# Kernel tuning notes

Hardware: AMD Instinct MI355X
Metric: run time of the kernel (lower is better)

## Reference

```python
import jax, jax.numpy as jnp
import numpy as np

H = 256  # GRU hidden size
V = 56   # decoder vocab / fc1 out


def gru_cell(x, h, wih, whh, bih, bhh):
    # PyTorch GRU cell math (gate order: r, z, n)
    gi = x @ wih.T + bih
    gh = h @ whh.T + bhh
    ir, iz, inn = jnp.split(gi, 3, axis=-1)
    hr, hz, hn = jnp.split(gh, 3, axis=-1)
    r = jax.nn.sigmoid(ir + hr)
    z = jax.nn.sigmoid(iz + hz)
    n = jnp.tanh(inn + r * hn)
    return (1.0 - z) * n + z * h


def gru_scan(seq, h0, wih, whh, bih, bhh):
    def step(h, xt):
        h = gru_cell(xt, h, wih, whh, bih, bhh)
        return h, h
    hT, ys = jax.lax.scan(step, h0, seq)
    return ys, hT


def bigru(seq, pf, pb):
    # seq: (S, N, F). Returns (S, N, 2H), final fwd hidden (N,H), final bwd hidden (N,H)
    S, N, _ = seq.shape
    h0 = jnp.zeros((N, H), seq.dtype)
    yf, hf = gru_scan(seq, h0, *pf)
    yb_rev, hb = gru_scan(seq[::-1], h0, *pb)
    return jnp.concatenate([yf, yb_rev[::-1]], axis=-1), hf, hb


def setup_inputs() -> dict:
    key = jax.random.key(0)
    ks = iter(jax.random.split(key, 32))
    s = 0.05
    p = {}
    p["x"] = jax.random.normal(next(ks), (64, 48, 512, 2, 2), dtype=jnp.float32)
    # bi_gru_1: input 192
    for d in ("f", "b"):
        p[f"w_ih_1{d}"] = jax.random.normal(next(ks), (3 * H, 192), jnp.float32) * s
        p[f"w_hh_1{d}"] = jax.random.normal(next(ks), (3 * H, H), jnp.float32) * s
        p[f"b_ih_1{d}"] = jax.random.normal(next(ks), (3 * H,), jnp.float32) * s
        p[f"b_hh_1{d}"] = jax.random.normal(next(ks), (3 * H,), jnp.float32) * s
    # bi_gru_2: input 512
    for d in ("f", "b"):
        p[f"w_ih_2{d}"] = jax.random.normal(next(ks), (3 * H, 2 * H), jnp.float32) * s
        p[f"w_hh_2{d}"] = jax.random.normal(next(ks), (3 * H, H), jnp.float32) * s
        p[f"b_ih_2{d}"] = jax.random.normal(next(ks), (3 * H,), jnp.float32) * s
        p[f"b_hh_2{d}"] = jax.random.normal(next(ks), (3 * H,), jnp.float32) * s
    # decoder GRU: input 56
    p["w_ih_d"] = jax.random.normal(next(ks), (3 * H, V), jnp.float32) * s
    p["w_hh_d"] = jax.random.normal(next(ks), (3 * H, H), jnp.float32) * s
    p["b_ih_d"] = jax.random.normal(next(ks), (3 * H,), jnp.float32) * s
    p["b_hh_d"] = jax.random.normal(next(ks), (3 * H,), jnp.float32) * s
    p["w_fc1"] = jax.random.normal(next(ks), (V, H), jnp.float32) * s
    p["b_fc1"] = jax.random.normal(next(ks), (V,), jnp.float32) * s
    p["w_adj"] = jax.random.normal(next(ks), (H, 2 * H), jnp.float32) * s
    p["b_adj"] = jax.random.normal(next(ks), (H,), jnp.float32) * s
    p["target_length"] = 6
    return p


def reference(x,
              w_ih_1f, w_hh_1f, b_ih_1f, b_hh_1f,
              w_ih_1b, w_hh_1b, b_ih_1b, b_hh_1b,
              w_ih_2f, w_hh_2f, b_ih_2f, b_hh_2f,
              w_ih_2b, w_hh_2b, b_ih_2b, b_hh_2b,
              w_ih_d, w_hh_d, b_ih_d, b_hh_d,
              w_fc1, b_fc1, w_adj, b_adj,
              target_length):
    B, C, T, Hh, Ww = x.shape
    # permute(2,0,1,3,4).contiguous().view(B, T, -1): flat buffer in (T,B,..) order reshaped to (B,T,feat)
    seq = jnp.transpose(x, (2, 0, 1, 3, 4)).reshape(B, T, C * Hh * Ww)
    # GRUs run seq-first: seq dim = B, batch dim = T (faithful to the torch code)
    y1, _, _ = bigru(seq, (w_ih_1f, w_hh_1f, b_ih_1f, b_hh_1f),
                     (w_ih_1b, w_hh_1b, b_ih_1b, b_hh_1b))
    # dropout is identity at inference
    y2, hf, hb = bigru(y1, (w_ih_2f, w_hh_2f, b_ih_2f, b_hh_2f),
                       (w_ih_2b, w_hh_2b, b_ih_2b, b_hh_2b))
    combined = jnp.concatenate([hf, hb], axis=-1)       # (T, 2H)
    dec_h_all = combined @ w_adj.T + b_adj              # (T, H)
    dec_h = dec_h_all[:B]                               # loop over b in range(B) selects first B rows
    inp0 = jnp.zeros((B, V), x.dtype)

    def step(carry, _):
        inp, h = carry
        h = gru_cell(inp, h, w_ih_d, w_hh_d, b_ih_d, b_hh_d)
        out = h @ w_fc1.T + b_fc1
        return (out, h), out

    _, outs = jax.lax.scan(step, (inp0, dec_h), None, length=target_length)
    return jnp.transpose(outs, (1, 0, 2))  # (B, target_length, V)
```

## Files before the change

### kernel.cpp

```cpp
#include <hip/hip_runtime.h>
#include <hip/hip_fp16.h>
#include <stdint.h>


#define HD 256
#define G3 768
#define NSEQ 64
#define NSTEP 64

typedef _Float16 hvec2 __attribute__((ext_vector_type(2)));
typedef _Float16 f16x8 __attribute__((ext_vector_type(8)));
typedef float f32x4 __attribute__((ext_vector_type(4)));

__device__ __forceinline__ float sigmf(float x) {
    return 1.0f / (1.0f + __expf(-x));
}

#if __has_builtin(__builtin_amdgcn_fdot2)
__device__ __forceinline__ float fdot2u(uint32_t w, uint32_t h, float acc) {
    return __builtin_amdgcn_fdot2(__builtin_bit_cast(hvec2, w),
                                  __builtin_bit_cast(hvec2, h), acc, false);
}
#else
__device__ __forceinline__ float fdot2u(uint32_t w, uint32_t h, float acc) {
    const __half2 wv = __builtin_bit_cast(__half2, w);
    const __half2 hv = __builtin_bit_cast(__half2, h);
    acc += __half2float(wv.x) * __half2float(hv.x);
    acc += __half2float(wv.y) * __half2float(hv.y);
    return acc;
}
#endif

__device__ __forceinline__ uint32_t pkh(float a, float b) {
    uint32_t lo = __half_as_ushort(__float2half_rn(a));
    uint32_t hi = __half_as_ushort(__float2half_rn(b));
    return lo | (hi << 16);
}

#define L8(X) X(0) X(1) X(2) X(3) X(4) X(5) X(6) X(7)

#define LRES(i) \
    const uint4 wr##i = wbase[(i) * G3]; \
    const uint4 wz##i = wbase[(i) * G3 + 256]; \
    const uint4 wn##i = wbase[(i) * G3 + 512];

#define DRES(i) { \
    const uint4 hp = *(const uint4*)&hb[hoff + 4 * (i)]; \
    ar0 = fdot2u(wr##i.x, hp.x, ar0); ar1 = fdot2u(wr##i.y, hp.y, ar1); \
    ar0 = fdot2u(wr##i.z, hp.z, ar0); ar1 = fdot2u(wr##i.w, hp.w, ar1); \
    az0 = fdot2u(wz##i.x, hp.x, az0); az1 = fdot2u(wz##i.y, hp.y, az1); \
    az0 = fdot2u(wz##i.z, hp.z, az0); az1 = fdot2u(wz##i.w, hp.w, az1); \
    an0 = fdot2u(wn##i.x, hp.x, an0); an1 = fdot2u(wn##i.y, hp.y, an1); \
    an0 = fdot2u(wn##i.z, hp.z, an0); an1 = fdot2u(wn##i.w, hp.w, an1); }

__global__ __launch_bounds__(256) void prep_all(
    const float* __restrict__ whh1f, const float* __restrict__ whh1b,
    const float* __restrict__ whh2f, const float* __restrict__ whh2b,
    const float* __restrict__ whhd,
    uint32_t* __restrict__ wt1f, uint32_t* __restrict__ wt1b,
    uint32_t* __restrict__ wt2f, uint32_t* __restrict__ wt2b,
    uint32_t* __restrict__ wtd,
    const float* __restrict__ wih1f, const float* __restrict__ wih1b,
    const float* __restrict__ wih2f, const float* __restrict__ wih2b,
    __half* __restrict__ wih1f_h, __half* __restrict__ wih1b_h,
    __half* __restrict__ wih2f_h, __half* __restrict__ wih2b_h,
    const float* __restrict__ wihd, const float* __restrict__ wadj,
    const float* __restrict__ wfc1,
    float* __restrict__ wihdT, float* __restrict__ wadjT,
    float* __restrict__ wfc1T,
    const float* __restrict__ x, __half* __restrict__ seqg)
{
    const int b   = blockIdx.x;
    const int tid = threadIdx.x;

    if (b < 480) {
        const int y = b / 96;
        const float* w; uint32_t* o;
        switch (y) {
            case 0: w = whh1f; o = wt1f; break;
            case 1: w = whh1b; o = wt1b; break;
            case 2: w = whh2f; o = wt2f; break;
            case 3: w = whh2b; o = wt2b; break;
            default: w = whhd; o = wtd; break;
        }
        const int idx = (b % 96) * 256 + tid;
        const int j = idx >> 5, q = idx & 31;
        const float4 fa = *(const float4*)(w + j * HD + 8 * q);
        const float4 fb = *(const float4*)(w + j * HD + 8 * q + 4);
        uint4 r;
        r.x = pkh(fa.x, fa.y); r.y = pkh(fa.z, fa.w);
        r.z = pkh(fb.x, fb.y); r.w = pkh(fb.z, fb.w);
        ((uint4*)o)[q * G3 + j] = r;
    } else if (b < 1536) {
        const float* s; __half* d; int i4;
        if (b < 624)       { s = wih1f; d = wih1f_h; i4 = (b - 480) * 256 + tid; }
        else if (b < 768)  { s = wih1b; d = wih1b_h; i4 = (b - 624) * 256 + tid; }
        else if (b < 1152) { s = wih2f; d = wih2f_h; i4 = (b - 768) * 256 + tid; }
        else               { s = wih2b; d = wih2b_h; i4 = (b - 1152) * 256 + tid; }
        const float4 v = *(const float4*)(s + (size_t)i4 * 4);
        __half2 lo; lo.x = __float2half_rn(v.x); lo.y = __float2half_rn(v.y);
        __half2 hi; hi.x = __float2half_rn(v.z); hi.y = __float2half_rn(v.w);
        *(__half2*)(d + (size_t)i4 * 4)     = lo;
        *(__half2*)(d + (size_t)i4 * 4 + 2) = hi;
    } else if (b < 2272) {
        const int idx = (b - 1536) * 256 + tid;
        if (idx < 43008) {
            int v = idx / G3, j = idx % G3;
            wihdT[idx] = wihd[j * 56 + v];
        } else if (idx < 43008 + 131072) {
            int i2 = idx - 43008;
            int f = i2 / HD, i = i2 % HD;
            wadjT[i2] = wadj[i * 512 + f];
        } else {
            int i3 = idx - 174080;
            int k = i3 / 56, v = i3 % 56;
            wfc1T[i3] = wfc1[v * HD + k];
        }
    } else {
        const int idx = (b - 2272) * 256 + tid;
        const int f = idx % 192;
        const int m = idx / 192;
        const int n = m >> 6, s = m & 63;
        seqg[idx] = __float2half(
            x[n * 98304 + (f >> 2) * 2048 + s * 32 + (f & 3)]);
    }
}

__global__ __launch_bounds__(256) void gemm_mfma(
    const __half* __restrict__ A,
    const __half* __restrict__ B0, const __half* __restrict__ B1,
    const float* __restrict__ bias0, const float* __restrict__ bias1,
    float* __restrict__ C0, float* __restrict__ C1, int K)
{
    const __half* B    = blockIdx.z ? B1 : B0;
    const float*  bias = blockIdx.z ? bias1 : bias0;
    float*        C    = blockIdx.z ? C1 : C0;
    const int m0 = blockIdx.x * 64;
    const int n0 = blockIdx.y * 64;
    const int w  = threadIdx.x >> 6;
    const int l  = threadIdx.x & 63;
    const int lr = l & 15;
    const int lk = (l >> 4) * 8;

    const __half* arow = A + (size_t)(m0 + w * 16 + lr) * K + lk;
    const __half* brow = B + (size_t)(n0 + lr) * K + lk;

    f32x4 acc0 = {0.f, 0.f, 0.f, 0.f};
    f32x4 acc1 = acc0, acc2 = acc0, acc3 = acc0;

#pragma unroll 2
    for (int k0 = 0; k0 < K; k0 += 32) {
        const f16x8 a  = *(const f16x8*)(arow + k0);
        const f16x8 b0 = *(const f16x8*)(brow + k0);
        const f16x8 b1 = *(const f16x8*)(brow + 16 * K + k0);
        const f16x8 b2 = *(const f16x8*)(brow + 32 * K + k0);
        const f16x8 b3 = *(const f16x8*)(brow + 48 * K + k0);
        acc0 = __builtin_amdgcn_mfma_f32_16x16x32_f16(a, b0, acc0, 0, 0, 0);
        acc1 = __builtin_amdgcn_mfma_f32_16x16x32_f16(a, b1, acc1, 0, 0, 0);
        acc2 = __builtin_amdgcn_mfma_f32_16x16x32_f16(a, b2, acc2, 0, 0, 0);
        acc3 = __builtin_amdgcn_mfma_f32_16x16x32_f16(a, b3, acc3, 0, 0, 0);
    }

    const int crow = m0 + w * 16 + (l >> 4) * 4;
    const int ccol = n0 + lr;
    float* cp = C + (size_t)crow * G3 + ccol;
    const float bb0 = bias[ccol];
    const float bb1 = bias[ccol + 16];
    const float bb2 = bias[ccol + 32];
    const float bb3 = bias[ccol + 48];
#pragma unroll
    for (int j = 0; j < 4; ++j) {
        cp[(size_t)j * G3 +  0] = acc0[j] + bb0;
        cp[(size_t)j * G3 + 16] = acc1[j] + bb1;
        cp[(size_t)j * G3 + 32] = acc2[j] + bb2;
        cp[(size_t)j * G3 + 48] = acc3[j] + bb3;
    }
}

__global__ __launch_bounds__(512, 1) void gru_scan(
    const float* __restrict__ giF, const float* __restrict__ giB,
    const uint32_t* __restrict__ wTF, const uint32_t* __restrict__ wTB,
    const float* __restrict__ bhhF, const float* __restrict__ bhhB,
    __half* __restrict__ y1h, float* __restrict__ hfin)
{
    const int dir = blockIdx.x & 1;
    const int n   = blockIdx.x >> 1;
    const int t   = threadIdx.x;
    const int tr  = t & 255;
    const int kh  = t >> 8;
    const int hoff = kh * 64;
    const float* gi  = dir ? giB : giF;
    const float* bhh = dir ? bhhB : bhhF;
    const uint4* wbase = (const uint4*)(dir ? wTB : wTF) + (size_t)(kh * 16) * G3 + tr;

    __shared__ __align__(16) uint32_t h1u[2][HD / 2];
    __shared__ float ph_r[HD], ph_z[HD], ph_n[HD];
    __shared__ float gin[2][G3];

    L8(LRES)
    const float bhr = bhh[tr], bhz = bhh[256 + tr], bhn = bhh[512 + tr];

    const float* gbase = gi + (size_t)n * NSTEP * G3;
    const int s0 = dir ? (NSTEP - 1) : 0;
#pragma unroll
    for (int i = t; i < G3; i += 512) gin[0][i] = gbase[s0 * G3 + i];

    float h_own = 0.0f;
    if (t < HD / 2) h1u[0][t] = 0u;
    __syncthreads();

    int s = s0;
    for (int step = 0; step < NSTEP; ++step) {
        const uint32_t* hb = h1u[step & 1];
        float ar0 = 0.f, ar1 = 0.f;
        float az0 = 0.f, az1 = 0.f;
        float an0 = 0.f, an1 = 0.f;
        L8(DRES)
#pragma unroll
        for (int i = 8; i < 16; ++i) {
            const uint4 sr = wbase[i * G3];
            const uint4 sz = wbase[i * G3 + 256];
            const uint4 sn = wbase[i * G3 + 512];
            const uint4 hp = *(const uint4*)&hb[hoff + 4 * i];
            ar0 = fdot2u(sr.x, hp.x, ar0); ar1 = fdot2u(sr.y, hp.y, ar1);
            ar0 = fdot2u(sr.z, hp.z, ar0); ar1 = fdot2u(sr.w, hp.w, ar1);
            az0 = fdot2u(sz.x, hp.x, az0); az1 = fdot2u(sz.y, hp.y, az1);
            az0 = fdot2u(sz.z, hp.z, az0); az1 = fdot2u(sz.w, hp.w, az1);
            an0 = fdot2u(sn.x, hp.x, an0); an1 = fdot2u(sn.y, hp.y, an1);
            an0 = fdot2u(sn.z, hp.z, an0); an1 = fdot2u(sn.w, hp.w, an1);
        }

        if (kh) {
            ph_r[tr] = ar0 + ar1;
            ph_z[tr] = az0 + az1;
            ph_n[tr] = an0 + an1;
        }
        __syncthreads();
        const int s_nxt = dir ? (step < NSTEP - 1 ? NSTEP - 2 - step : 0)
                              : (step < NSTEP - 1 ? step + 1 : NSTEP - 1);
        if (kh == 0) {
            const float* gcur = gin[step & 1];
            const float ghr = (ar0 + ar1) + ph_r[tr] + bhr;
            const float ghz = (az0 + az1) + ph_z[tr] + bhz;
            const float ghn = (an0 + an1) + ph_n[tr] + bhn;
            const float r  = sigmf(gcur[tr] + ghr);
            const float z  = sigmf(gcur[256 + tr] + ghz);
            const float nn = tanhf(gcur[512 + tr] + r * ghn);
            const float hnew = (1.0f - z) * nn + z * h_own;
            h_own = hnew;
            const __half hh = __float2half(hnew);
            ((__half*)h1u[(step + 1) & 1])[tr] = hh;
            y1h[(size_t)(n * NSTEP + s) * 512 + dir * HD + tr] = hh;
        } else {
            float* gnxt = gin[(step + 1) & 1];
#pragma unroll
            for (int i = tr; i < G3; i += 256)
                gnxt[i] = gbase[s_nxt * G3 + i];
        }
        s = s_nxt;
        __syncthreads();
    }
    if (kh == 0)
        hfin[(size_t)(dir * NSEQ + n) * HD + tr] = h_own;
}

__global__ __launch_bounds__(256) void adj_kernel(
    const float* __restrict__ hfin, const float* __restrict__ wadjT,
    const float* __restrict__ badj, float* __restrict__ dech)
{
    const int n = blockIdx.x, t = threadIdx.x;
    __shared__ float comb[512];
    comb[t]      = hfin[(size_t)n * HD + t];
    comb[HD + t] = hfin[(size_t)(NSEQ + n) * HD + t];
    __syncthreads();
    float acc = badj[t];
#pragma unroll 8
    for (int f = 0; f < 512; ++f) acc += wadjT[f * HD + t] * comb[f];
    dech[n * HD + t] = acc;
}

__global__ __launch_bounds__(768, 3) void decoder_kernel(
    const float* __restrict__ dech, const uint32_t* __restrict__ wTd,
    const float* __restrict__ wihdT, const float* __restrict__ bihd,
    const float* __restrict__ bhhd, const float* __restrict__ wfc1T,
    const float* __restrict__ bfc1, float* __restrict__ out)
{
    const int n = blockIdx.x, t = threadIdx.x;
    const uint4* wq = (const uint4*)wTd + t;

    __shared__ __align__(16) uint32_t h1u[2][HD / 2];
    __shared__ float ghs[G3], gis[G3];
    __shared__ float hfp[HD];
    __shared__ float inp[56];
    __shared__ float pf1[448];

    const float bi = bihd[t], bh = bhhd[t];

    float h_own = 0.0f;
    if (t < HD) {
        const float hv = dech[(size_t)n * HD + t];
        h_own = hv;
        ((__half*)h1u[0])[t] = __float2half(hv);
        hfp[t] = hv;
    }
    if (t < 56) inp[t] = 0.0f;
    __syncthreads();

    for (int step = 0; step < 6; ++step) {
        const uint32_t* hb = h1u[step & 1];
        float a0 = 0.f, a1 = 0.f;
#pragma unroll 8
        for (int q = 0; q < 32; ++q) {
            const uint4 w = wq[q * G3];
            const uint4 hp = *(const uint4*)&hb[4 * q];
            a0 = fdot2u(w.x, hp.x, a0); a1 = fdot2u(w.y, hp.y, a1);
            a0 = fdot2u(w.z, hp.z, a0); a1 = fdot2u(w.w, hp.w, a1);
        }
        float ai = bi;
#pragma unroll 8
        for (int v = 0; v < 56; ++v) ai += wihdT[v * G3 + t] * inp[v];
        ghs[t] = a0 + a1 + bh;
        gis[t] = ai;
        __syncthreads();
        if (t < HD) {
            const float r  = sigmf(gis[t] + ghs[t]);
            const float z  = sigmf(gis[HD + t] + ghs[HD + t]);
            const float nn = tanhf(gis[2 * HD + t] + r * ghs[2 * HD + t]);
            const float hnew = (1.0f - z) * nn + z * h_own;
            h_own = hnew;
            ((__half*)h1u[(step + 1) & 1])[t] = __float2half(hnew);
            hfp[t] = hnew;
        }
        __syncthreads();
        if (t < 448) {
            const int v = t >> 3, g = t & 7;
            float o = 0.f;
#pragma unroll
            for (int k2 = 0; k2 < 32; ++k2)
                o += wfc1T[(g * 32 + k2) * 56 + v] * hfp[g * 32 + k2];
            pf1[t] = o;
        }
        __syncthreads();
        if (t < 56) {
            float o = bfc1[t];
#pragma unroll
            for (int g = 0; g < 8; ++g) o += pf1[t * 8 + g];
            out[(size_t)n * 336 + step * 56 + t] = o;
            inp[t] = o;
        }
        __syncthreads();
    }
}

extern "C" void kernel_launch(void* const* d_in, const int* in_sizes, int n_in,
                              void* d_out, int out_size, void* d_ws, size_t ws_size,
                              hipStream_t stream)
{
    const float* x      = (const float*)d_in[0];
    const float* wih1f  = (const float*)d_in[1];
    const float* whh1f  = (const float*)d_in[2];
    const float* bih1f  = (const float*)d_in[3];
    const float* bhh1f  = (const float*)d_in[4];
    const float* wih1b  = (const float*)d_in[5];
    const float* whh1b  = (const float*)d_in[6];
    const float* bih1b  = (const float*)d_in[7];
    const float* bhh1b  = (const float*)d_in[8];
    const float* wih2f  = (const float*)d_in[9];
    const float* whh2f  = (const float*)d_in[10];
    const float* bih2f  = (const float*)d_in[11];
    const float* bhh2f  = (const float*)d_in[12];
    const float* wih2b  = (const float*)d_in[13];
    const float* whh2b  = (const float*)d_in[14];
    const float* bih2b  = (const float*)d_in[15];
    const float* bhh2b  = (const float*)d_in[16];
    const float* wihd   = (const float*)d_in[17];
    const float* whhd   = (const float*)d_in[18];
    const float* bihd   = (const float*)d_in[19];
    const float* bhhd   = (const float*)d_in[20];
    const float* wfc1   = (const float*)d_in[21];
    const float* bfc1   = (const float*)d_in[22];
    const float* wadj   = (const float*)d_in[23];
    const float* badj   = (const float*)d_in[24];

    float* ws = (float*)d_ws;
    __half*   seqg_h  = (__half*)(ws + 0);
    float*    gi_f    = ws + 393216;
    float*    gi_b    = ws + 3538944;
    __half*   y1h     = (__half*)(ws + 6684672);
    float*    hfin    = ws + 7733248;
    float*    dech    = ws + 7766016;
    uint32_t* wt1f    = (uint32_t*)(ws + 7782400);
    uint32_t* wt1b    = (uint32_t*)(ws + 7880704);
    uint32_t* wt2f    = (uint32_t*)(ws + 7979008);
    uint32_t* wt2b    = (uint32_t*)(ws + 8077312);
    uint32_t* wtd     = (uint32_t*)(ws + 8175616);
    __half*   wih1f_h = (__half*)(ws + 8273920);
    __half*   wih1b_h = (__half*)(ws + 8347648);
    __half*   wih2f_h = (__half*)(ws + 8421376);
    __half*   wih2b_h = (__half*)(ws + 8617984);
    float*    wihdT   = ws + 8814592;
    float*    wadjT   = ws + 8857600;
    float*    wfc1T   = ws + 8988672;

    prep_all<<<5344, 256, 0, stream>>>(
        whh1f, whh1b, whh2f, whh2b, whhd,
        wt1f, wt1b, wt2f, wt2b, wtd,
        wih1f, wih1b, wih2f, wih2b,
        wih1f_h, wih1b_h, wih2f_h, wih2b_h,
        wihd, wadj, wfc1, wihdT, wadjT, wfc1T,
        x, seqg_h);

    gemm_mfma<<<dim3(64, 12, 2), 256, 0, stream>>>(
        seqg_h, wih1f_h, wih1b_h, bih1f, bih1b, gi_f, gi_b, 192);
    gru_scan<<<128, 512, 0, stream>>>(
        gi_f, gi_b, wt1f, wt1b, bhh1f, bhh1b, y1h, hfin);

    gemm_mfma<<<dim3(64, 12, 2), 256, 0, stream>>>(
        y1h, wih2f_h, wih2b_h, bih2f, bih2b, gi_f, gi_b, 512);
    gru_scan<<<128, 512, 0, stream>>>(
        gi_f, gi_b, wt2f, wt2b, bhh2f, bhh2b, y1h, hfin);

    adj_kernel<<<64, 256, 0, stream>>>(hfin, wadjT, badj, dech);
    decoder_kernel<<<64, 768, 0, stream>>>(
        dech, wtd, wihdT, bihd, bhhd, wfc1T, bfc1, (float*)d_out);
}
```

Before: 355.5 us.

## Split GRU recurrent dot across four thread groups and fuse adj into decoder

```diff
diff --git a/kernel.cpp b/kernel.cpp
--- a/kernel.cpp
+++ b/kernel.cpp
@@ -37,7 +37,7 @@
     return lo | (hi << 16);
 }
 
-#define L8(X) X(0) X(1) X(2) X(3) X(4) X(5) X(6) X(7)
+#define L5(X) X(0) X(1) X(2) X(3) X(4)
 
 #define LRES(i) \
     const uint4 wr##i = wbase[(i) * G3]; \
@@ -177,7 +177,7 @@
     }
 }
 
-__global__ __launch_bounds__(512, 1) void gru_scan(
+__global__ __launch_bounds__(1024, 1) void gru_scan(
     const float* __restrict__ giF, const float* __restrict__ giB,
     const uint32_t* __restrict__ wTF, const uint32_t* __restrict__ wTB,
     const float* __restrict__ bhhF, const float* __restrict__ bhhB,
@@ -187,23 +187,23 @@
     const int n   = blockIdx.x >> 1;
     const int t   = threadIdx.x;
     const int tr  = t & 255;
-    const int kh  = t >> 8;
-    const int hoff = kh * 64;
+    const int kq  = t >> 8;
+    const int hoff = kq * 32;
     const float* gi  = dir ? giB : giF;
     const float* bhh = dir ? bhhB : bhhF;
-    const uint4* wbase = (const uint4*)(dir ? wTB : wTF) + (size_t)(kh * 16) * G3 + tr;
+    const uint4* wbase = (const uint4*)(dir ? wTB : wTF)
+                       + (size_t)(kq * 8) * G3 + tr;
 
     __shared__ __align__(16) uint32_t h1u[2][HD / 2];
-    __shared__ float ph_r[HD], ph_z[HD], ph_n[HD];
+    __shared__ float ph_r[3 * HD], ph_z[3 * HD], ph_n[3 * HD];
     __shared__ float gin[2][G3];
 
-    L8(LRES)
+    L5(LRES)
     const float bhr = bhh[tr], bhz = bhh[256 + tr], bhn = bhh[512 + tr];
 
     const float* gbase = gi + (size_t)n * NSTEP * G3;
     const int s0 = dir ? (NSTEP - 1) : 0;
-#pragma unroll
-    for (int i = t; i < G3; i += 512) gin[0][i] = gbase[s0 * G3 + i];
+    if (t < G3) gin[0][t] = gbase[s0 * G3 + t];
 
     float h_own = 0.0f;
     if (t < HD / 2) h1u[0][t] = 0u;
@@ -215,9 +215,9 @@
         float ar0 = 0.f, ar1 = 0.f;
         float az0 = 0.f, az1 = 0.f;
         float an0 = 0.f, an1 = 0.f;
-        L8(DRES)
+        L5(DRES)
 #pragma unroll
-        for (int i = 8; i < 16; ++i) {
+        for (int i = 5; i < 8; ++i) {
             const uint4 sr = wbase[i * G3];
             const uint4 sz = wbase[i * G3 + 256];
             const uint4 sn = wbase[i * G3 + 512];
@@ -230,19 +230,22 @@
             an0 = fdot2u(sn.z, hp.z, an0); an1 = fdot2u(sn.w, hp.w, an1);
         }
 
-        if (kh) {
-            ph_r[tr] = ar0 + ar1;
-            ph_z[tr] = az0 + az1;
-            ph_n[tr] = an0 + an1;
+        if (kq) {
+            ph_r[(kq - 1) * HD + tr] = ar0 + ar1;
+            ph_z[(kq - 1) * HD + tr] = az0 + az1;
+            ph_n[(kq - 1) * HD + tr] = an0 + an1;
         }
         __syncthreads();
         const int s_nxt = dir ? (step < NSTEP - 1 ? NSTEP - 2 - step : 0)
                               : (step < NSTEP - 1 ? step + 1 : NSTEP - 1);
-        if (kh == 0) {
+        if (kq == 0) {
             const float* gcur = gin[step & 1];
-            const float ghr = (ar0 + ar1) + ph_r[tr] + bhr;
-            const float ghz = (az0 + az1) + ph_z[tr] + bhz;
-            const float ghn = (an0 + an1) + ph_n[tr] + bhn;
+            const float ghr = (ar0 + ar1) + ph_r[tr] + ph_r[HD + tr]
+                            + ph_r[2 * HD + tr] + bhr;
+            const float ghz = (az0 + az1) + ph_z[tr] + ph_z[HD + tr]
+                            + ph_z[2 * HD + tr] + bhz;
+            const float ghn = (an0 + an1) + ph_n[tr] + ph_n[HD + tr]
+                            + ph_n[2 * HD + tr] + bhn;
             const float r  = sigmf(gcur[tr] + ghr);
             const float z  = sigmf(gcur[256 + tr] + ghz);
             const float nn = tanhf(gcur[512 + tr] + r * ghn);
@@ -251,36 +254,22 @@
             const __half hh = __float2half(hnew);
             ((__half*)h1u[(step + 1) & 1])[tr] = hh;
             y1h[(size_t)(n * NSTEP + s) * 512 + dir * HD + tr] = hh;
-        } else {
+        } else if (kq == 1) {
             float* gnxt = gin[(step + 1) & 1];
-#pragma unroll
-            for (int i = tr; i < G3; i += 256)
-                gnxt[i] = gbase[s_nxt * G3 + i];
+            gnxt[tr]       = gbase[s_nxt * G3 + tr];
+            gnxt[256 + tr] = gbase[s_nxt * G3 + 256 + tr];
+            gnxt[512 + tr] = gbase[s_nxt * G3 + 512 + tr];
         }
         s = s_nxt;
         __syncthreads();
     }
-    if (kh == 0)
+    if (kq == 0)
         hfin[(size_t)(dir * NSEQ + n) * HD + tr] = h_own;
 }
 
-__global__ __launch_bounds__(256) void adj_kernel(
+__global__ __launch_bounds__(768, 3) void decoder_kernel(
     const float* __restrict__ hfin, const float* __restrict__ wadjT,
-    const float* __restrict__ badj, float* __restrict__ dech)
-{
-    const int n = blockIdx.x, t = threadIdx.x;
-    __shared__ float comb[512];
-    comb[t]      = hfin[(size_t)n * HD + t];
-    comb[HD + t] = hfin[(size_t)(NSEQ + n) * HD + t];
-    __syncthreads();
-    float acc = badj[t];
-#pragma unroll 8
-    for (int f = 0; f < 512; ++f) acc += wadjT[f * HD + t] * comb[f];
-    dech[n * HD + t] = acc;
-}
-
-__global__ __launch_bounds__(768, 3) void decoder_kernel(
-    const float* __restrict__ dech, const uint32_t* __restrict__ wTd,
+    const float* __restrict__ badj, const uint32_t* __restrict__ wTd,
     const float* __restrict__ wihdT, const float* __restrict__ bihd,
     const float* __restrict__ bhhd, const float* __restrict__ wfc1T,
     const float* __restrict__ bfc1, float* __restrict__ out)
@@ -289,6 +278,7 @@
     const uint4* wq = (const uint4*)wTd + t;
 
     __shared__ __align__(16) uint32_t h1u[2][HD / 2];
+    __shared__ float comb[512];
     __shared__ float ghs[G3], gis[G3];
     __shared__ float hfp[HD];
     __shared__ float inp[56];
@@ -296,14 +286,21 @@
 
     const float bi = bihd[t], bh = bhhd[t];
 
+    if (t < 512)
+        comb[t] = (t < 256) ? hfin[(size_t)n * HD + t]
+                            : hfin[(size_t)(NSEQ + n) * HD + (t - 256)];
+    if (t < 56) inp[t] = 0.0f;
+    __syncthreads();
+
     float h_own = 0.0f;
     if (t < HD) {
-        const float hv = dech[(size_t)n * HD + t];
-        h_own = hv;
-        ((__half*)h1u[0])[t] = __float2half(hv);
-        hfp[t] = hv;
-    }
-    if (t < 56) inp[t] = 0.0f;
+        float acc = badj[t];
+#pragma unroll 8
+        for (int f = 0; f < 512; ++f) acc += wadjT[f * HD + t] * comb[f];
+        h_own = acc;
+        ((__half*)h1u[0])[t] = __float2half(acc);
+        hfp[t] = acc;
+    }
     __syncthreads();
 
     for (int step = 0; step < 6; ++step) {
@@ -388,7 +385,6 @@
     float*    gi_b    = ws + 3538944;
     __half*   y1h     = (__half*)(ws + 6684672);
     float*    hfin    = ws + 7733248;
-    float*    dech    = ws + 7766016;
     uint32_t* wt1f    = (uint32_t*)(ws + 7782400);
     uint32_t* wt1b    = (uint32_t*)(ws + 7880704);
     uint32_t* wt2f    = (uint32_t*)(ws + 7979008);
@@ -412,15 +408,15 @@
 
     gemm_mfma<<<dim3(64, 12, 2), 256, 0, stream>>>(
         seqg_h, wih1f_h, wih1b_h, bih1f, bih1b, gi_f, gi_b, 192);
-    gru_scan<<<128, 512, 0, stream>>>(
+    gru_scan<<<128, 1024, 0, stream>>>(
         gi_f, gi_b, wt1f, wt1b, bhh1f, bhh1b, y1h, hfin);
 
     gemm_mfma<<<dim3(64, 12, 2), 256, 0, stream>>>(
         y1h, wih2f_h, wih2b_h, bih2f, bih2b, gi_f, gi_b, 512);
-    gru_scan<<<128, 512, 0, stream>>>(
+    gru_scan<<<128, 1024, 0, stream>>>(
         gi_f, gi_b, wt2f, wt2b, bhh2f, bhh2b, y1h, hfin);
 
-    adj_kernel<<<64, 256, 0, stream>>>(hfin, wadjT, badj, dech);
     decoder_kernel<<<64, 768, 0, stream>>>(
-        dech, wtd, wihdT, bihd, bhhd, wfc1T, bfc1, (float*)d_out);
-}
+        hfin, wadjT, badj, wtd, wihdT, bihd, bhhd, wfc1T, bfc1,
+        (float*)d_out);
+}
```

After: 398.4 us. +12.1%, slower.
